# Optimization experiments

Hardware: AMD Instinct MI355X
Metric: run time of the kernel (lower is better)

## Reference

```python
import jax, jax.numpy as jnp
import numpy as np

B, S, D, H = 1, 2048, 1024, 16
HD = D // H
DFF = 4 * D
EPS = 1e-5


def _layernorm(x, g, b):
    mu = jnp.mean(x, axis=-1, keepdims=True)
    var = jnp.mean(jnp.square(x - mu), axis=-1, keepdims=True)
    return (x - mu) * jax.lax.rsqrt(var + EPS) * g + b


def setup_inputs() -> dict:
    key = jax.random.key(0)
    ks = jax.random.split(key, 8)
    scale = 1.0 / np.sqrt(D)
    # standard ALiBi slopes: 2^(-8*i/H)
    slopes = jnp.asarray(2.0 ** (-8.0 * (np.arange(1, H + 1) / H)), dtype=jnp.float32)
    return {
        "x": jax.random.normal(ks[0], (B, S, D), jnp.float32),
        "alibi_slopes": slopes,
        "wq": jax.random.normal(ks[1], (D, D), jnp.float32) * scale,
        "wk": jax.random.normal(ks[2], (D, D), jnp.float32) * scale,
        "wv": jax.random.normal(ks[3], (D, D), jnp.float32) * scale,
        "wo": jax.random.normal(ks[4], (D, D), jnp.float32) * scale,
        "ff1_w": jax.random.normal(ks[5], (DFF, D), jnp.float32) * scale,
        "ff1_b": jnp.zeros((DFF,), jnp.float32),
        "ff2_w": jax.random.normal(ks[6], (D, DFF), jnp.float32) * (1.0 / np.sqrt(DFF)),
        "ff2_b": jnp.zeros((D,), jnp.float32),
        "ln1_g": jnp.ones((D,), jnp.float32),
        "ln1_b": jnp.zeros((D,), jnp.float32),
        "ln2_g": jnp.ones((D,), jnp.float32),
        "ln2_b": jnp.zeros((D,), jnp.float32),
    }


def reference(x, alibi_slopes, wq, wk, wv, wo, ff1_w, ff1_b, ff2_w, ff2_b,
              ln1_g, ln1_b, ln2_g, ln2_b):
    b, s, d = x.shape
    residual = x
    h = _layernorm(x, ln1_g, ln1_b)
    # projections (torch Linear: y = x @ W^T); split heads
    q = (h @ wq.T).reshape(b, s, H, HD)
    k = (h @ wk.T).reshape(b, s, H, HD)
    v = (h @ wv.T).reshape(b, s, H, HD)
    scores = jnp.einsum("bqhd,bkhd->bhqk", q, k) / np.sqrt(HD)  # [B,H,S,S]
    # ALiBi: distance[i,j] = j - i; scores -= slope * distance
    pos = jnp.arange(s, dtype=jnp.float32)
    dist = pos[None, :] - pos[:, None]                    # [S,S]
    scores = scores - alibi_slopes[None, :, None, None] * dist[None, None]
    # causal mask (query i attends to keys j <= i)
    causal = pos[:, None] >= pos[None, :]
    scores = jnp.where(causal[None, None], scores, -jnp.inf)
    attn = jax.nn.softmax(scores, axis=-1)
    out = jnp.einsum("bhqk,bkhd->bqhd", attn, v).reshape(b, s, d)
    out = out @ wo.T
    x = residual + out
    residual = x
    h2 = _layernorm(x, ln2_g, ln2_b)
    ff = jax.nn.gelu(h2 @ ff1_w.T + ff1_b, approximate=False) @ ff2_w.T + ff2_b
    return residual + ff
```

## Files before the change

kernel.cpp:

```cpp
#include <hip/hip_runtime.h>
#include <math.h>

typedef unsigned short u16;
typedef __bf16 bf16x8 __attribute__((ext_vector_type(8)));
typedef float f32x4 __attribute__((ext_vector_type(4)));
typedef u16 u16x4 __attribute__((ext_vector_type(4)));
typedef u16 u16x8 __attribute__((ext_vector_type(8)));

#define DEV __device__ __forceinline__

DEV u16 f2bf(float f) {
  unsigned u = __builtin_bit_cast(unsigned, f);
  u += 0x7FFFu + ((u >> 16) & 1u);
  return (u16)(u >> 16);
}
DEV float bf2f(u16 b) {
  unsigned u = ((unsigned)b) << 16;
  return __builtin_bit_cast(float, u);
}

DEV void gload16(const void* g, void* l) {
  __builtin_amdgcn_global_load_lds((__attribute__((address_space(1))) void*)g,
                                   (__attribute__((address_space(3))) void*)l, 16, 0, 0);
}

__launch_bounds__(256)
__global__ void prep(const float* __restrict__ x, const float* __restrict__ gam,
                     const float* __restrict__ bet, u16* __restrict__ hout,
                     const float* __restrict__ wq, const float* __restrict__ wk,
                     const float* __restrict__ wv, const float* __restrict__ wo,
                     const float* __restrict__ f1, const float* __restrict__ f2,
                     u16* __restrict__ dq, u16* __restrict__ dk, u16* __restrict__ dv,
                     u16* __restrict__ dwo, u16* __restrict__ df1, u16* __restrict__ df2) {
  int t = threadIdx.x;
  if (blockIdx.x < 2048) {
    int row = blockIdx.x;
    float4 v = ((const float4*)(x + (size_t)row * 1024))[t];
    float s = v.x + v.y + v.z + v.w;
    float s2 = v.x * v.x + v.y * v.y + v.z * v.z + v.w * v.w;
    for (int off = 1; off < 64; off <<= 1) {
      s += __shfl_xor(s, off);
      s2 += __shfl_xor(s2, off);
    }
    __shared__ float red[8];
    int wv0 = t >> 6, ln = t & 63;
    if (ln == 0) { red[wv0] = s; red[wv0 + 4] = s2; }
    __syncthreads();
    s = red[0] + red[1] + red[2] + red[3];
    s2 = red[4] + red[5] + red[6] + red[7];
    float mu = s * (1.f / 1024.f);
    float var = s2 * (1.f / 1024.f) - mu * mu;
    float rs = rsqrtf(var + 1e-5f);
    float4 gv = ((const float4*)gam)[t];
    float4 bv = ((const float4*)bet)[t];
    u16x4 o = { f2bf((v.x - mu) * rs * gv.x + bv.x), f2bf((v.y - mu) * rs * gv.y + bv.y),
                f2bf((v.z - mu) * rs * gv.z + bv.z), f2bf((v.w - mu) * rs * gv.w + bv.w) };
    ((u16x4*)(hout + (size_t)row * 1024))[t] = o;
  } else {
    int i = (blockIdx.x - 2048) * 256 + t;
    const float* src;
    u16* dst;
    int local;
    if (i < (1 << 18)) { src = wq; dst = dq; local = i; }
    else if (i < (2 << 18)) { src = wk; dst = dk; local = i - (1 << 18); }
    else if (i < (3 << 18)) { src = wv; dst = dv; local = i - (2 << 18); }
    else if (i < (4 << 18)) { src = wo; dst = dwo; local = i - (3 << 18); }
    else if (i < (4 << 18) + (1 << 20)) { src = f1; dst = df1; local = i - (4 << 18); }
    else { src = f2; dst = df2; local = i - ((4 << 18) + (1 << 20)); }
    float4 v = ((const float4*)src)[local];
    u16x4 o = { f2bf(v.x), f2bf(v.y), f2bf(v.z), f2bf(v.w) };
    ((u16x4*)dst)[local] = o;
  }
}

__launch_bounds__(256)
__global__ void ln2_add(const float* __restrict__ x, const float* __restrict__ P0,
                        const float* __restrict__ P1, const float* __restrict__ gam,
                        const float* __restrict__ bet, float* __restrict__ x2,
                        u16* __restrict__ out) {
  int row = blockIdx.x;
  int t = threadIdx.x;
  size_t base = (size_t)row * 256 + t;
  float4 xv = ((const float4*)x)[base];
  float4 p0 = ((const float4*)P0)[base];
  float4 p1 = ((const float4*)P1)[base];
  float4 v = { xv.x + p0.x + p1.x, xv.y + p0.y + p1.y,
               xv.z + p0.z + p1.z, xv.w + p0.w + p1.w };
  ((float4*)x2)[base] = v;
  float s = v.x + v.y + v.z + v.w;
  float s2 = v.x * v.x + v.y * v.y + v.z * v.z + v.w * v.w;
  for (int off = 1; off < 64; off <<= 1) {
    s += __shfl_xor(s, off);
    s2 += __shfl_xor(s2, off);
  }
  __shared__ float red[8];
  int wv = t >> 6, ln = t & 63;
  if (ln == 0) { red[wv] = s; red[wv + 4] = s2; }
  __syncthreads();
  s = red[0] + red[1] + red[2] + red[3];
  s2 = red[4] + red[5] + red[6] + red[7];
  float mu = s * (1.f / 1024.f);
  float var = s2 * (1.f / 1024.f) - mu * mu;
  float rs = rsqrtf(var + 1e-5f);
  float4 gv = ((const float4*)gam)[t];
  float4 bv = ((const float4*)bet)[t];
  u16x4 o = { f2bf((v.x - mu) * rs * gv.x + bv.x), f2bf((v.y - mu) * rs * gv.y + bv.y),
              f2bf((v.z - mu) * rs * gv.z + bv.z), f2bf((v.w - mu) * rs * gv.w + bv.w) };
  ((u16x4*)(out + (size_t)row * 1024))[t] = o;
}

__launch_bounds__(256)
__global__ void final_add(const float* __restrict__ x2, const float* __restrict__ b2,
                          const u16* __restrict__ Qp, size_t qoff,
                          float* __restrict__ out) {
  int row = blockIdx.x;
  int t = threadIdx.x;
  size_t base = (size_t)row * 256 + t;
  float4 xv = ((const float4*)x2)[base];
  float4 bv = ((const float4*)b2)[t];
  float4 o = { xv.x + bv.x, xv.y + bv.y, xv.z + bv.z, xv.w + bv.w };
#pragma unroll
  for (int i = 0; i < 4; ++i) {
    u16x4 q = ((const u16x4*)(Qp + i * qoff))[base];
    o.x += bf2f(q[0]);
    o.y += bf2f(q[1]);
    o.z += bf2f(q[2]);
    o.w += bf2f(q[3]);
  }
  ((float4*)out)[base] = o;
}

__launch_bounds__(256)
__global__ void transpose_v(const u16* __restrict__ V, u16* __restrict__ Vt) {
  const int st = blockIdx.x, h = blockIdx.y;
  __shared__ u16 tile[64][72];
  const int t = threadIdx.x;
  const int r = t >> 3, c8 = t & 7;
#pragma unroll
  for (int i = 0; i < 2; ++i) {
    int row = i * 32 + r;
    *(u16x8*)&tile[row][c8 * 8] =
        *(const u16x8*)&V[(size_t)(st * 64 + row) * 1024 + h * 64 + c8 * 8];
  }
  __syncthreads();
#pragma unroll
  for (int i = 0; i < 2; ++i) {
    int d = i * 32 + r;
    u16x8 o;
#pragma unroll
    for (int jj = 0; jj < 8; ++jj) o[jj] = tile[c8 * 8 + jj][d];
    *(u16x8*)&Vt[(size_t)(h * 64 + d) * 2048 + st * 64 + c8 * 8] = o;
  }
}

template <int BM, int BN, int WR, int WC, int EPI, int SPLITK, int SWZ>
__launch_bounds__(256, 2)
__global__ void gemm_bt(const u16* __restrict__ A, const u16* __restrict__ B,
                        void* __restrict__ C, const float* __restrict__ bias,
                        const float* __restrict__ resid, int M, int N, int K,
                        size_t zoff) {
  constexpr int FM = BM / WR / 16;
  constexpr int FN = BN / WC / 16;
  __shared__ u16 As[BM * 32];
  __shared__ u16 Bs[BN * 32];
  int bxi = blockIdx.x, byi = blockIdx.y, bzi = blockIdx.z;
  if constexpr (SWZ == 1) {
    int bid = bxi + 8 * (byi + (int)gridDim.y * bzi);
    int xcd = bid & 7, k = bid >> 3;
    bxi = xcd;
    byi = k % (int)gridDim.y;
    bzi = k / (int)gridDim.y;
  } else if constexpr (SWZ == 2) {
    int bid = bxi + 32 * blockIdx.y;
    int xcd = bid & 7, k = bid >> 3;
    bxi = xcd * 4 + (k & 3);
    byi = k >> 2;
    bzi = 0;
  }
  const int t = threadIdx.x, lane = t & 63, w = t >> 6;
  const int wr = w / WC, wc = w % WC;
  const int g = lane >> 4, l16 = lane & 15;
  const int m0 = byi * BM, n0 = bxi * BN;
  const int ks = K / SPLITK;
  const int k0 = (SPLITK > 1) ? bzi * ks : 0;
  const size_t cbase = (SPLITK > 1) ? (size_t)bzi * zoff : 0;
  f32x4 acc[FM][FN] = {};
  const int nkt = ks >> 5;
  for (int kt = 0; kt < nkt; ++kt) {
    const u16* Ag = A + (size_t)m0 * K + k0 + kt * 32;
    const u16* Bg = B + (size_t)n0 * K + k0 + kt * 32;
#pragma unroll
    for (int i = 0; i < BM / 64; ++i) {
      int c = i * 256 + t;
      gload16(Ag + (size_t)(c >> 2) * K + (c & 3) * 8, &As[(i * 256 + w * 64) * 8]);
    }
#pragma unroll
    for (int i = 0; i < BN / 64; ++i) {
      int c = i * 256 + t;
      gload16(Bg + (size_t)(c >> 2) * K + (c & 3) * 8, &Bs[(i * 256 + w * 64) * 8]);
    }
    __syncthreads();
    bf16x8 af[FM], bfr[FN];
#pragma unroll
    for (int m = 0; m < FM; ++m)
      af[m] = *(const bf16x8*)&As[(wr * FM * 16 + m * 16 + l16) * 32 + g * 8];
#pragma unroll
    for (int n = 0; n < FN; ++n)
      bfr[n] = *(const bf16x8*)&Bs[(wc * FN * 16 + n * 16 + l16) * 32 + g * 8];
#pragma unroll
    for (int m = 0; m < FM; ++m)
#pragma unroll
      for (int n = 0; n < FN; ++n)
        acc[m][n] = __builtin_amdgcn_mfma_f32_16x16x32_bf16(af[m], bfr[n], acc[m][n], 0, 0, 0);
    __syncthreads();
  }
#pragma unroll
  for (int m = 0; m < FM; ++m)
#pragma unroll
    for (int n = 0; n < FN; ++n)
#pragma unroll
      for (int r = 0; r < 4; ++r) {
        int row = m0 + wr * FM * 16 + m * 16 + g * 4 + r;
        int col = n0 + wc * FN * 16 + n * 16 + l16;
        size_t idx = (size_t)row * N + col;
        float v = acc[m][n][r];
        if constexpr (EPI == 0) {
          ((u16*)C)[cbase + idx] = f2bf(v);
        } else if constexpr (EPI == 1) {
          v += bias[col];
          v = 0.5f * v * (1.f + erff(v * 0.70710678118f));
          ((u16*)C)[idx] = f2bf(v);
        } else if constexpr (EPI == 2) {
          ((float*)C)[idx] = v + bias[col] + resid[idx];
        } else if constexpr (EPI == 3) {
          ((float*)C)[idx] = v + resid[idx];
        } else {
          ((float*)C)[cbase + idx] = v;
        }
      }
}

__launch_bounds__(256, 2)
__global__ void gemm_qkv64(const u16* __restrict__ A, const u16* __restrict__ B0,
                           const u16* __restrict__ B1, const u16* __restrict__ B2,
                           u16* __restrict__ C0, u16* __restrict__ C1, u16* __restrict__ C2) {
  constexpr int FM = 4, FN = 2;
  const int K = 1024, N = 1024;
  int bid = blockIdx.x + 24 * blockIdx.y;
  int xcd = bid & 7, kk0 = bid >> 3;
  const int bxs = xcd * 3 + kk0 % 3;
  const int bys = kk0 / 3;
  const int which = bxs >> 3;
  const u16* B = which == 0 ? B0 : which == 1 ? B1 : B2;
  u16* C = which == 0 ? C0 : which == 1 ? C1 : C2;
  __shared__ u16 As[64 * 32];
  __shared__ u16 Bs[128 * 32];
  const int t = threadIdx.x, lane = t & 63, w = t >> 6;
  const int wc = w;
  const int g = lane >> 4, l16 = lane & 15;
  const int m0 = bys * 64, n0 = (bxs & 7) * 128;
  f32x4 acc[FM][FN] = {};
  for (int kt = 0; kt < 32; ++kt) {
    const u16* Ag = A + (size_t)m0 * K + kt * 32;
    const u16* Bg = B + (size_t)n0 * K + kt * 32;
    {
      int c = t;
      gload16(Ag + (size_t)(c >> 2) * K + (c & 3) * 8, &As[(w * 64) * 8]);
    }
#pragma unroll
    for (int i = 0; i < 2; ++i) {
      int c = i * 256 + t;
      gload16(Bg + (size_t)(c >> 2) * K + (c & 3) * 8, &Bs[(i * 256 + w * 64) * 8]);
    }
    __syncthreads();
    bf16x8 af[FM], bfr[FN];
#pragma unroll
    for (int m = 0; m < FM; ++m)
      af[m] = *(const bf16x8*)&As[(m * 16 + l16) * 32 + g * 8];
#pragma unroll
    for (int n = 0; n < FN; ++n)
      bfr[n] = *(const bf16x8*)&Bs[(wc * FN * 16 + n * 16 + l16) * 32 + g * 8];
#pragma unroll
    for (int m = 0; m < FM; ++m)
#pragma unroll
      for (int n = 0; n < FN; ++n)
        acc[m][n] = __builtin_amdgcn_mfma_f32_16x16x32_bf16(af[m], bfr[n], acc[m][n], 0, 0, 0);
    __syncthreads();
  }
#pragma unroll
  for (int m = 0; m < FM; ++m)
#pragma unroll
    for (int n = 0; n < FN; ++n)
#pragma unroll
      for (int r = 0; r < 4; ++r) {
        int row = m0 + m * 16 + g * 4 + r;
        int col = n0 + wc * FN * 16 + n * 16 + l16;
        C[(size_t)row * N + col] = f2bf(acc[m][n][r]);
      }
}

__launch_bounds__(256, 4)
__global__ void attn_fwd(const u16* __restrict__ Q, const u16* __restrict__ Kb,
                         const u16* __restrict__ Vt, const float* __restrict__ slopes,
                         u16* __restrict__ O, float* __restrict__ BoG,
                         float* __restrict__ BlG) {
  const int p = blockIdx.x;
  const int h = blockIdx.y;
  const int z = blockIdx.z;
  const int t = threadIdx.x, lane = t & 63, w = t >> 6;
  const int g = lane >> 4, l16 = lane & 15;
  const float slope = slopes[h];
  const int TA = p + 1;
  const int qbB = 31 - p;

  __shared__ u16 Ks[2][4096];
  __shared__ u16 Vs[2][4096];
  __shared__ u16 Ps[4][16][72];

  const int r0 = w * 8 + (lane >> 3), r1 = 32 + r0;
  const int c8 = lane & 7;
  const int c0s = c8 ^ (r0 & 7), c1s = c8 ^ (r1 & 7);
  const int sw = l16 & 7;
  const u16x8 ones_u = { 0x3F80, 0x3F80, 0x3F80, 0x3F80, 0x3F80, 0x3F80, 0x3F80, 0x3F80 };
  const bf16x8 ones = __builtin_bit_cast(bf16x8, ones_u);

  auto stage = [&](int buf, int kv0) {
    gload16(Kb + (size_t)(kv0 + r0) * 1024 + h * 64 + c0s * 8, &Ks[buf][(w * 64) * 8]);
    gload16(Kb + (size_t)(kv0 + r1) * 1024 + h * 64 + c1s * 8, &Ks[buf][(256 + w * 64) * 8]);
    gload16(Vt + (size_t)(h * 64 + r0) * 2048 + kv0 + c0s * 8, &Vs[buf][(w * 64) * 8]);
    gload16(Vt + (size_t)(h * 64 + r1) * 2048 + kv0 + c1s * 8, &Vs[buf][(256 + w * 64) * 8]);
  };
  auto kvOf = [&](int idx) { return idx < TA ? idx * 64 : (idx - TA) * 64; };

  const int myStart = z * 17;
  const int myEnd = z ? 33 : 17;

  int qb = (z == 0) ? p : qbB;
  int q0 = qb * 64 + w * 16;
  bf16x8 qf[2];
#pragma unroll
  for (int kk = 0; kk < 2; ++kk)
    qf[kk] = *(const bf16x8*)&Q[(size_t)(q0 + l16) * 1024 + h * 64 + kk * 32 + g * 8];
  f32x4 o_acc[4] = {};
  f32x4 lsum = {};

  stage(0, kvOf(myStart));
  __syncthreads();

  int cur = 0;
  for (int it = 0; it < 17; ++it) {
    const int idx = myStart + it;
    const bool active = idx < myEnd;
    if (z == 0 && idx == TA) {
#pragma unroll
      for (int d = 0; d < 4; ++d)
#pragma unroll
        for (int r = 0; r < 4; ++r) {
          int row = q0 + g * 4 + r;
          O[(size_t)row * 1024 + h * 64 + d * 16 + l16] = f2bf(o_acc[d][r] / lsum[r]);
        }
      qb = qbB;
      q0 = qb * 64 + w * 16;
#pragma unroll
      for (int kk = 0; kk < 2; ++kk)
        qf[kk] = *(const bf16x8*)&Q[(size_t)(q0 + l16) * 1024 + h * 64 + kk * 32 + g * 8];
#pragma unroll
      for (int d = 0; d < 4; ++d) o_acc[d] = f32x4{};
      lsum = f32x4{};
    }
    if (idx + 1 < myEnd) stage(cur ^ 1, kvOf(idx + 1));
    if (active) {
      const int kv0 = kvOf(idx);
      const bool lastT = (idx == TA - 1) || (idx == 32);
      f32x4 s[4];
      __builtin_amdgcn_s_setprio(1);
#pragma unroll
      for (int n = 0; n < 4; ++n) {
        bf16x8 kf0 = *(const bf16x8*)&Ks[cur][(n * 16 + l16) * 64 + ((g ^ sw) * 8)];
        bf16x8 kf1 = *(const bf16x8*)&Ks[cur][(n * 16 + l16) * 64 + (((4 + g) ^ sw) * 8)];
        f32x4 z4 = {};
        s[n] = __builtin_amdgcn_mfma_f32_16x16x32_bf16(qf[0], kf0, z4, 0, 0, 0);
        s[n] = __builtin_amdgcn_mfma_f32_16x16x32_bf16(qf[1], kf1, s[n], 0, 0, 0);
      }
      __builtin_amdgcn_s_setprio(0);
      const float aB = -slope * (float)(kv0 + l16);
#pragma unroll
      for (int n = 0; n < 4; ++n) {
        const float aN = aB - slope * (float)(n * 16);
        const int kj = kv0 + n * 16 + l16;
        u16x4 pr;
#pragma unroll
        for (int r = 0; r < 4; ++r) {
          float val = fmaf(s[n][r], 0.125f, aN);
          if (lastT) {
            int qi = q0 + g * 4 + r;
            val = (kj <= qi) ? val : -1e30f;
          }
          pr[r] = f2bf(__expf(val));
        }
#pragma unroll
        for (int r = 0; r < 4; ++r) Ps[w][g * 4 + r][n * 16 + l16] = pr[r];
      }
      bf16x8 pf[2];
#pragma unroll
      for (int kk = 0; kk < 2; ++kk)
        pf[kk] = *(const bf16x8*)&Ps[w][l16][kk * 32 + g * 8];
      __builtin_amdgcn_s_setprio(1);
#pragma unroll
      for (int kk = 0; kk < 2; ++kk)
        lsum = __builtin_amdgcn_mfma_f32_16x16x32_bf16(pf[kk], ones, lsum, 0, 0, 0);
#pragma unroll
      for (int d = 0; d < 4; ++d) {
#pragma unroll
        for (int kk = 0; kk < 2; ++kk) {
          bf16x8 vv = *(const bf16x8*)&Vs[cur][(d * 16 + l16) * 64 + (((kk * 4 + g) ^ sw) * 8)];
          o_acc[d] = __builtin_amdgcn_mfma_f32_16x16x32_bf16(pf[kk], vv, o_acc[d], 0, 0, 0);
        }
      }
      __builtin_amdgcn_s_setprio(0);
    }
    __syncthreads();
    cur ^= 1;
  }
  const size_t slot = ((size_t)p * 16 + h) * 2 + z;
  float* Bo = BoG + slot * 4096;
  float* Bl = BlG + slot * 64;
#pragma unroll
  for (int d = 0; d < 4; ++d)
#pragma unroll
    for (int r = 0; r < 4; ++r)
      Bo[(w * 16 + g * 4 + r) * 64 + d * 16 + l16] = o_acc[d][r];
  if (l16 == 0) {
#pragma unroll
    for (int r = 0; r < 4; ++r) Bl[w * 16 + g * 4 + r] = lsum[r];
  }
}

__launch_bounds__(256)
__global__ void merge_b(const float* __restrict__ BoG, const float* __restrict__ BlG,
                        u16* __restrict__ O) {
  const int p = blockIdx.x, h = blockIdx.y;
  const int qbB = 31 - p;
  const size_t s0 = (((size_t)p * 16 + h) * 2 + 0);
  const size_t s1 = s0 + 1;
  const float* Bo0 = BoG + s0 * 4096;
  const float* Bo1 = BoG + s1 * 4096;
  const float* Bl0 = BlG + s0 * 64;
  const float* Bl1 = BlG + s1 * 64;
  const int t = threadIdx.x;
#pragma unroll
  for (int i = 0; i < 4; ++i) {
    int idx = t + i * 256;
    int row = idx >> 4, c4 = idx & 15;
    float inv = 1.f / (Bl0[row] + Bl1[row]);
    float4 a = ((const float4*)Bo0)[(size_t)row * 16 + c4];
    float4 b = ((const float4*)Bo1)[(size_t)row * 16 + c4];
    u16x4 o = { f2bf((a.x + b.x) * inv), f2bf((a.y + b.y) * inv),
                f2bf((a.z + b.z) * inv), f2bf((a.w + b.w) * inv) };
    *(u16x4*)&O[(size_t)(qbB * 64 + row) * 1024 + h * 64 + c4 * 4] = o;
  }
}

extern "C" void kernel_launch(void* const* d_in, const int* in_sizes, int n_in,
                              void* d_out, int out_size, void* d_ws, size_t ws_size,
                              hipStream_t stream) {
  const float* x = (const float*)d_in[0];
  const float* slopes = (const float*)d_in[1];
  const float* wq = (const float*)d_in[2];
  const float* wk = (const float*)d_in[3];
  const float* wv = (const float*)d_in[4];
  const float* wo = (const float*)d_in[5];
  const float* ff1w = (const float*)d_in[6];
  const float* ff1b = (const float*)d_in[7];
  const float* ff2w = (const float*)d_in[8];
  const float* ff2b = (const float*)d_in[9];
  const float* ln1g = (const float*)d_in[10];
  const float* ln1b = (const float*)d_in[11];
  const float* ln2g = (const float*)d_in[12];
  const float* ln2b = (const float*)d_in[13];
  float* out = (float*)d_out;

  if (ws_size < (size_t)(56u << 20)) return;

  char* ws = (char*)d_ws;
  u16* hbuf = (u16*)(ws + 0);
  u16* Qb = (u16*)(ws + (4u << 20));
  u16* Kbf = (u16*)(ws + (8u << 20));
  u16* Vbf = (u16*)(ws + (12u << 20));
  u16* Vtb = (u16*)(ws + (16u << 20));
  float* P0 = (float*)(ws + (4u << 20));
  float* P1 = (float*)(ws + (12u << 20));
  u16* ffact = Qb;
  float* x2 = (float*)(ws + (20u << 20));
  float* BoG = (float*)(ws + (20u << 20));
  u16* h2 = (u16*)(ws + (28u << 20));
  float* BlG = (float*)(ws + (28u << 20));
  u16* wqb = (u16*)(ws + (32u << 20));
  u16* wkb = (u16*)(ws + (34u << 20));
  u16* wvb = (u16*)(ws + (36u << 20));
  u16* wob = (u16*)(ws + (38u << 20));
  u16* ff1wb = (u16*)(ws + (40u << 20));
  u16* ff2wb = (u16*)(ws + (48u << 20));
  u16* attnO = hbuf;
  u16* Qp = (u16*)(ws + (32u << 20));
  const size_t q4off = (size_t)(4u << 20) / 2;

  prep<<<2048 + 12288, 256, 0, stream>>>(x, ln1g, ln1b, hbuf, wq, wk, wv, wo, ff1w, ff2w,
                                         wqb, wkb, wvb, wob, ff1wb, ff2wb);
  gemm_qkv64<<<dim3(24, 32), 256, 0, stream>>>(hbuf, wqb, wkb, wvb, Qb, Kbf, Vbf);
  transpose_v<<<dim3(32, 16), 256, 0, stream>>>(Vbf, Vtb);
  attn_fwd<<<dim3(16, 16, 2), 256, 0, stream>>>(Qb, Kbf, Vtb, slopes, attnO, BoG, BlG);
  merge_b<<<dim3(16, 16), 256, 0, stream>>>(BoG, BlG, attnO);
  gemm_bt<64, 128, 1, 4, 4, 2, 1><<<dim3(8, 32, 2), 256, 0, stream>>>(
      attnO, wob, P0, nullptr, nullptr, 2048, 1024, 1024, (size_t)2048 * 1024);
  ln2_add<<<2048, 256, 0, stream>>>(x, P0, P1, ln2g, ln2b, x2, h2);
  gemm_bt<128, 128, 2, 2, 1, 1, 2><<<dim3(32, 16), 256, 0, stream>>>(
      h2, ff1wb, ffact, ff1b, nullptr, 2048, 4096, 1024, 0);
  gemm_bt<64, 128, 1, 4, 0, 4, 1><<<dim3(8, 32, 4), 256, 0, stream>>>(
      ffact, ff2wb, Qp, nullptr, nullptr, 2048, 1024, 4096, q4off);
  final_add<<<2048, 256, 0, stream>>>(x2, ff2b, Qp, q4off, out);
}
```

Measured before the change: 174.1 us.

## Split attention KV range three ways and use bf16 split-K partials for Wo

Attention work per (pair, head) is now split across three blocks of 11 KV tiles each instead of two blocks of 17. All partial outputs, including the first query block's, are written as unnormalised bf16 slots and reduced by a rewritten merge kernel. The Wo projection moves to a 4-way split-K GEMM that writes bf16 partials, which ln2_add sums. The aim is more blocks to fill the CUs and less partial-buffer traffic. In exchange it adds extra merge reads and zero-fill writes, and loses some accuracy because partial sums are stored in bf16.

Measured after the change: 171.1 us. About the same (-1.8%).

```diff
diff --git a/kernel.cpp b/kernel.cpp
--- a/kernel.cpp
+++ b/kernel.cpp
@@ -74,18 +74,22 @@
 }
 
 __launch_bounds__(256)
-__global__ void ln2_add(const float* __restrict__ x, const float* __restrict__ P0,
-                        const float* __restrict__ P1, const float* __restrict__ gam,
+__global__ void ln2_add(const float* __restrict__ x, const u16* __restrict__ Pw,
+                        size_t poff, const float* __restrict__ gam,
                         const float* __restrict__ bet, float* __restrict__ x2,
                         u16* __restrict__ out) {
   int row = blockIdx.x;
   int t = threadIdx.x;
   size_t base = (size_t)row * 256 + t;
-  float4 xv = ((const float4*)x)[base];
-  float4 p0 = ((const float4*)P0)[base];
-  float4 p1 = ((const float4*)P1)[base];
-  float4 v = { xv.x + p0.x + p1.x, xv.y + p0.y + p1.y,
-               xv.z + p0.z + p1.z, xv.w + p0.w + p1.w };
+  float4 v = ((const float4*)x)[base];
+#pragma unroll
+  for (int i = 0; i < 4; ++i) {
+    u16x4 q = ((const u16x4*)(Pw + i * poff))[base];
+    v.x += bf2f(q[0]);
+    v.y += bf2f(q[1]);
+    v.z += bf2f(q[2]);
+    v.w += bf2f(q[3]);
+  }
   ((float4*)x2)[base] = v;
   float s = v.x + v.y + v.z + v.w;
   float s2 = v.x * v.x + v.y * v.y + v.z * v.z + v.w * v.w;
@@ -302,7 +306,7 @@
 __launch_bounds__(256, 4)
 __global__ void attn_fwd(const u16* __restrict__ Q, const u16* __restrict__ Kb,
                          const u16* __restrict__ Vt, const float* __restrict__ slopes,
-                         u16* __restrict__ O, float* __restrict__ BoG,
+                         u16* __restrict__ BoLo, u16* __restrict__ BoHi,
                          float* __restrict__ BlG) {
   const int p = blockIdx.x;
   const int h = blockIdx.y;
@@ -331,34 +335,48 @@
     gload16(Vt + (size_t)(h * 64 + r1) * 2048 + kv0 + c1s * 8, &Vs[buf][(256 + w * 64) * 8]);
   };
   auto kvOf = [&](int idx) { return idx < TA ? idx * 64 : (idx - TA) * 64; };
-
-  const int myStart = z * 17;
-  const int myEnd = z ? 33 : 17;
-
-  int qb = (z == 0) ? p : qbB;
+  auto boPtr = [&](size_t slot) {
+    return slot < 1024 ? BoLo + slot * 4096 : BoHi + (slot - 1024) * 4096;
+  };
+
+  const int myStart = z * 11;
+  const int myEnd = myStart + 11;
+  const size_t slotBase = (((size_t)p * 16 + h) * 3 + z) * 2;
+
+  bool flushed[2] = { false, false };
+  f32x4 o_acc[4] = {};
+  f32x4 lsum = {};
+
+  auto flush = [&](int c) {
+    u16* Bo = boPtr(slotBase + c);
+    float* Bl = BlG + (slotBase + c) * 64;
+#pragma unroll
+    for (int d = 0; d < 4; ++d)
+#pragma unroll
+      for (int r = 0; r < 4; ++r)
+        Bo[(w * 16 + g * 4 + r) * 64 + d * 16 + l16] = f2bf(o_acc[d][r]);
+    if (l16 == 0) {
+#pragma unroll
+      for (int r = 0; r < 4; ++r) Bl[w * 16 + g * 4 + r] = lsum[r];
+    }
+    flushed[c] = true;
+  };
+
+  int qb = (myStart < TA) ? p : qbB;
   int q0 = qb * 64 + w * 16;
   bf16x8 qf[2];
 #pragma unroll
   for (int kk = 0; kk < 2; ++kk)
     qf[kk] = *(const bf16x8*)&Q[(size_t)(q0 + l16) * 1024 + h * 64 + kk * 32 + g * 8];
-  f32x4 o_acc[4] = {};
-  f32x4 lsum = {};
 
   stage(0, kvOf(myStart));
   __syncthreads();
 
   int cur = 0;
-  for (int it = 0; it < 17; ++it) {
+  for (int it = 0; it < 11; ++it) {
     const int idx = myStart + it;
-    const bool active = idx < myEnd;
-    if (z == 0 && idx == TA) {
-#pragma unroll
-      for (int d = 0; d < 4; ++d)
-#pragma unroll
-        for (int r = 0; r < 4; ++r) {
-          int row = q0 + g * 4 + r;
-          O[(size_t)row * 1024 + h * 64 + d * 16 + l16] = f2bf(o_acc[d][r] / lsum[r]);
-        }
+    if (idx == TA && myStart < TA) {
+      flush(0);
       qb = qbB;
       q0 = qb * 64 + w * 16;
 #pragma unroll
@@ -368,8 +386,8 @@
       for (int d = 0; d < 4; ++d) o_acc[d] = f32x4{};
       lsum = f32x4{};
     }
-    if (idx + 1 < myEnd) stage(cur ^ 1, kvOf(idx + 1));
-    if (active) {
+    if (it + 1 < 11) stage(cur ^ 1, kvOf(idx + 1));
+    {
       const int kv0 = kvOf(idx);
       const bool lastT = (idx == TA - 1) || (idx == 32);
       f32x4 s[4];
@@ -422,42 +440,51 @@
     __syncthreads();
     cur ^= 1;
   }
-  const size_t slot = ((size_t)p * 16 + h) * 2 + z;
-  float* Bo = BoG + slot * 4096;
-  float* Bl = BlG + slot * 64;
-#pragma unroll
-  for (int d = 0; d < 4; ++d)
-#pragma unroll
-    for (int r = 0; r < 4; ++r)
-      Bo[(w * 16 + g * 4 + r) * 64 + d * 16 + l16] = o_acc[d][r];
-  if (l16 == 0) {
-#pragma unroll
-    for (int r = 0; r < 4; ++r) Bl[w * 16 + g * 4 + r] = lsum[r];
-  }
+  flush((myEnd - 1) < TA ? 0 : 1);
+#pragma unroll
+  for (int c = 0; c < 2; ++c)
+    if (!flushed[c]) {
+      u16* Bo = boPtr(slotBase + c);
+      float* Bl = BlG + (slotBase + c) * 64;
+#pragma unroll
+      for (int i = 0; i < 16; ++i) Bo[i * 256 + t] = 0;
+      if (t < 64) Bl[t] = 0.f;
+    }
 }
 
 __launch_bounds__(256)
-__global__ void merge_b(const float* __restrict__ BoG, const float* __restrict__ BlG,
-                        u16* __restrict__ O) {
+__global__ void merge_b(const u16* __restrict__ BoLo, const u16* __restrict__ BoHi,
+                        const float* __restrict__ BlG, u16* __restrict__ O) {
   const int p = blockIdx.x, h = blockIdx.y;
-  const int qbB = 31 - p;
-  const size_t s0 = (((size_t)p * 16 + h) * 2 + 0);
-  const size_t s1 = s0 + 1;
-  const float* Bo0 = BoG + s0 * 4096;
-  const float* Bo1 = BoG + s1 * 4096;
-  const float* Bl0 = BlG + s0 * 64;
-  const float* Bl1 = BlG + s1 * 64;
   const int t = threadIdx.x;
-#pragma unroll
-  for (int i = 0; i < 4; ++i) {
-    int idx = t + i * 256;
-    int row = idx >> 4, c4 = idx & 15;
-    float inv = 1.f / (Bl0[row] + Bl1[row]);
-    float4 a = ((const float4*)Bo0)[(size_t)row * 16 + c4];
-    float4 b = ((const float4*)Bo1)[(size_t)row * 16 + c4];
-    u16x4 o = { f2bf((a.x + b.x) * inv), f2bf((a.y + b.y) * inv),
-                f2bf((a.z + b.z) * inv), f2bf((a.w + b.w) * inv) };
-    *(u16x4*)&O[(size_t)(qbB * 64 + row) * 1024 + h * 64 + c4 * 4] = o;
+  const int row = t >> 2, c0 = (t & 3) * 16;
+  const size_t base = ((size_t)p * 16 + h) * 6;
+#pragma unroll
+  for (int c = 0; c < 2; ++c) {
+    const int qb = c == 0 ? p : 31 - p;
+    float l = 0.f;
+    float acc[16];
+#pragma unroll
+    for (int i = 0; i < 16; ++i) acc[i] = 0.f;
+#pragma unroll
+    for (int z = 0; z < 3; ++z) {
+      const size_t slot = base + (size_t)z * 2 + c;
+      l += BlG[slot * 64 + row];
+      const u16* Bo = (slot < 1024 ? BoLo + slot * 4096 : BoHi + (slot - 1024) * 4096) +
+                      row * 64 + c0;
+#pragma unroll
+      for (int i = 0; i < 16; ++i) acc[i] += bf2f(Bo[i]);
+    }
+    float inv = 1.f / l;
+    u16x8 o0, o1;
+#pragma unroll
+    for (int i = 0; i < 8; ++i) {
+      o0[i] = f2bf(acc[i] * inv);
+      o1[i] = f2bf(acc[8 + i] * inv);
+    }
+    u16* dst = O + (size_t)(qb * 64 + row) * 1024 + h * 64 + c0;
+    *(u16x8*)dst = o0;
+    *(u16x8*)(dst + 8) = o1;
   }
 }
 
@@ -488,13 +515,13 @@
   u16* Kbf = (u16*)(ws + (8u << 20));
   u16* Vbf = (u16*)(ws + (12u << 20));
   u16* Vtb = (u16*)(ws + (16u << 20));
-  float* P0 = (float*)(ws + (4u << 20));
-  float* P1 = (float*)(ws + (12u << 20));
+  u16* Pw = (u16*)(ws + (4u << 20));
   u16* ffact = Qb;
+  u16* BoLo = (u16*)(ws + (20u << 20));
+  u16* BoHi = (u16*)(ws + (12u << 20));
   float* x2 = (float*)(ws + (20u << 20));
-  float* BoG = (float*)(ws + (20u << 20));
+  float* BlG = (float*)(ws + (28u << 20));
   u16* h2 = (u16*)(ws + (28u << 20));
-  float* BlG = (float*)(ws + (28u << 20));
   u16* wqb = (u16*)(ws + (32u << 20));
   u16* wkb = (u16*)(ws + (34u << 20));
   u16* wvb = (u16*)(ws + (36u << 20));
@@ -504,16 +531,17 @@
   u16* attnO = hbuf;
   u16* Qp = (u16*)(ws + (32u << 20));
   const size_t q4off = (size_t)(4u << 20) / 2;
+  const size_t woff = (size_t)2048 * 1024;
 
   prep<<<2048 + 12288, 256, 0, stream>>>(x, ln1g, ln1b, hbuf, wq, wk, wv, wo, ff1w, ff2w,
                                          wqb, wkb, wvb, wob, ff1wb, ff2wb);
   gemm_qkv64<<<dim3(24, 32), 256, 0, stream>>>(hbuf, wqb, wkb, wvb, Qb, Kbf, Vbf);
   transpose_v<<<dim3(32, 16), 256, 0, stream>>>(Vbf, Vtb);
-  attn_fwd<<<dim3(16, 16, 2), 256, 0, stream>>>(Qb, Kbf, Vtb, slopes, attnO, BoG, BlG);
-  merge_b<<<dim3(16, 16), 256, 0, stream>>>(BoG, BlG, attnO);
-  gemm_bt<64, 128, 1, 4, 4, 2, 1><<<dim3(8, 32, 2), 256, 0, stream>>>(
-      attnO, wob, P0, nullptr, nullptr, 2048, 1024, 1024, (size_t)2048 * 1024);
-  ln2_add<<<2048, 256, 0, stream>>>(x, P0, P1, ln2g, ln2b, x2, h2);
+  attn_fwd<<<dim3(16, 16, 3), 256, 0, stream>>>(Qb, Kbf, Vtb, slopes, BoLo, BoHi, BlG);
+  merge_b<<<dim3(16, 16), 256, 0, stream>>>(BoLo, BoHi, BlG, attnO);
+  gemm_bt<64, 128, 1, 4, 0, 4, 1><<<dim3(8, 32, 4), 256, 0, stream>>>(
+      attnO, wob, Pw, nullptr, nullptr, 2048, 1024, 1024, woff);
+  ln2_add<<<2048, 256, 0, stream>>>(x, Pw, woff, ln2g, ln2b, x2, h2);
   gemm_bt<128, 128, 2, 2, 1, 1, 2><<<dim3(32, 16), 256, 0, stream>>>(
       h2, ff1wb, ffact, ff1b, nullptr, 2048, 4096, 1024, 0);
   gemm_bt<64, 128, 1, 4, 0, 4, 1><<<dim3(8, 32, 4), 256, 0, stream>>>(
```
